# Optimization experiments

Hardware: AMD Instinct MI355X
Metric: run time of the kernel (lower is better)

The kernel has to match this reference:

```python
import jax, jax.numpy as jnp
import numpy as np

N = 50000
E = 800000
IN, H, OUT = 128, 96, 64
BN_EPS = 1e-5


def setup_inputs() -> dict:
    key = jax.random.key(0)
    ks = jax.random.split(key, 16)
    x = jax.random.normal(ks[0], (N, IN), dtype=jnp.float32)
    edge_index = jax.random.randint(ks[1], (2, E), 0, N, dtype=jnp.int64)
    edge_weight = jax.random.uniform(ks[2], (E,), dtype=jnp.float32)
    def lin(k, fo, fi):
        # PyG glorot-ish init
        s = 1.0 / np.sqrt(fi)
        return jax.random.uniform(k, (fo, fi), minval=-s, maxval=s, dtype=jnp.float32)
    W1, b1 = lin(ks[3], H, IN), jnp.zeros((H,), jnp.float32)
    W2, b2 = lin(ks[4], H, H), jnp.zeros((H,), jnp.float32)
    W3, b3 = lin(ks[5], OUT, H), jnp.zeros((OUT,), jnp.float32)
    g1 = jnp.ones((H,), jnp.float32); beta1 = jnp.zeros((H,), jnp.float32)
    m1 = 0.1 * jax.random.normal(ks[6], (H,), dtype=jnp.float32)
    v1 = jnp.abs(1.0 + 0.1 * jax.random.normal(ks[7], (H,), dtype=jnp.float32))
    g2 = jnp.ones((H,), jnp.float32); beta2 = jnp.zeros((H,), jnp.float32)
    m2 = 0.1 * jax.random.normal(ks[8], (H,), dtype=jnp.float32)
    v2 = jnp.abs(1.0 + 0.1 * jax.random.normal(ks[9], (H,), dtype=jnp.float32))
    return dict(x=x, edge_index=edge_index, edge_weight=edge_weight,
                W1=W1, b1=b1, W2=W2, b2=b2, W3=W3, b3=b3,
                g1=g1, beta1=beta1, m1=m1, v1=v1,
                g2=g2, beta2=beta2, m2=m2, v2=v2)


def gcn_norm(edge_index, edge_weight, n):
    # PyG gcn_norm with add_self_loops=True, fill_value=1.0
    loop = jnp.arange(n, dtype=edge_index.dtype)
    row = jnp.concatenate([edge_index[0], loop])  # sources
    col = jnp.concatenate([edge_index[1], loop])  # targets
    ew = jnp.concatenate([edge_weight, jnp.ones((n,), edge_weight.dtype)])
    deg = jax.ops.segment_sum(ew, col, num_segments=n)
    dis = jnp.where(deg > 0, jax.lax.rsqrt(deg), 0.0)  # inf -> 0 masked_fill
    norm = dis[row] * ew * dis[col]
    return row, col, norm


def gcn_conv(x, row, col, norm, W, b, n):
    xw = x @ W.T                       # [N, F_out] dense transform first
    msg = norm[:, None] * xw[row]      # [E+N, F_out] gather + edge scale
    out = jax.ops.segment_sum(msg, col, num_segments=n)  # scatter-add
    return out + b


def bn_eval(x, gamma, beta, mean, var):
    return (x - mean) * jax.lax.rsqrt(var + BN_EPS) * gamma + beta


def reference(x, edge_index, edge_weight, W1, b1, W2, b2, W3, b3,
              g1, beta1, m1, v1, g2, beta2, m2, v2):
    n = x.shape[0]
    row, col, norm = gcn_norm(edge_index, edge_weight, n)  # cached=True: shared
    h = gcn_conv(x, row, col, norm, W1, b1, n)
    h = jax.nn.relu(bn_eval(h, g1, beta1, m1, v1))
    h = gcn_conv(h, row, col, norm, W2, b2, n)
    h = jax.nn.relu(bn_eval(h, g2, beta2, m2, v2))
    out = gcn_conv(h, row, col, norm, W3, b3, n)
    return out
```

## Files before the change

### kernel.cpp

```cpp
#include <hip/hip_runtime.h>
#include <hip/hip_fp16.h>


constexpr float BN_EPS = 1e-5f;
constexpr float DEG_SCALE = 131072.0f;
constexpr float INV_DEG_SCALE = 1.0f / 131072.0f;
constexpr float NORM_SCALE = 32768.0f;
constexpr float INV_NORM_SCALE = 1.0f / 32768.0f;

typedef _Float16 f16x8 __attribute__((ext_vector_type(8)));
typedef float f32x4 __attribute__((ext_vector_type(4)));


template <int K, int F, bool F32X, bool F32W>
__device__ __forceinline__ void gemm_block(const void* __restrict__ Xin,
                                           const void* __restrict__ Win,
                                           _Float16* __restrict__ Y,
                                           int n0b, int tid, int n,
                                           _Float16* lds) {
    constexpr int KT = K / 32;
    constexpr int FT = F / 16;
    constexpr int LROW = (F == 96) ? 104 : 72;
    int wave = tid >> 6;
    int lane = tid & 63;
    int quad = lane >> 4;
    int r = lane & 15;
    int n0 = n0b + wave * 16;
    bool active = (n0 < n);

    if (active) {
        f16x8 a[KT];
        if (F32X) {
            const float* xr = (const float*)Xin + (size_t)(n0 + r) * K + quad * 8;
#pragma unroll
            for (int kt = 0; kt < KT; ++kt) {
                float4 v0 = *(const float4*)(xr + kt * 32);
                float4 v1 = *(const float4*)(xr + kt * 32 + 4);
                f16x8 t = {(_Float16)v0.x, (_Float16)v0.y, (_Float16)v0.z, (_Float16)v0.w,
                           (_Float16)v1.x, (_Float16)v1.y, (_Float16)v1.z, (_Float16)v1.w};
                a[kt] = t;
            }
        } else {
            const f16x8* xr = (const f16x8*)((const _Float16*)Xin + (size_t)(n0 + r) * K + quad * 8);
#pragma unroll
            for (int kt = 0; kt < KT; ++kt) a[kt] = xr[kt * 4];
        }

        f32x4 acc[FT];
#pragma unroll
        for (int ft = 0; ft < FT; ++ft) acc[ft] = (f32x4){0.f, 0.f, 0.f, 0.f};

#pragma unroll
        for (int kt = 0; kt < KT; ++kt) {
#pragma unroll
            for (int ft = 0; ft < FT; ++ft) {
                f16x8 b;
                if (F32W) {
                    const float* wr = (const float*)Win + (size_t)(ft * 16 + r) * K + kt * 32 + quad * 8;
                    float4 v0 = *(const float4*)wr;
                    float4 v1 = *(const float4*)(wr + 4);
                    f16x8 t = {(_Float16)v0.x, (_Float16)v0.y, (_Float16)v0.z, (_Float16)v0.w,
                               (_Float16)v1.x, (_Float16)v1.y, (_Float16)v1.z, (_Float16)v1.w};
                    b = t;
                } else {
                    b = *(const f16x8*)((const _Float16*)Win + (size_t)(ft * 16 + r) * K + kt * 32 + quad * 8);
                }
                acc[ft] = __builtin_amdgcn_mfma_f32_16x16x32_f16(a[kt], b, acc[ft], 0, 0, 0);
            }
        }

#pragma unroll
        for (int ft = 0; ft < FT; ++ft) {
#pragma unroll
            for (int reg = 0; reg < 4; ++reg) {
                int lr = wave * 16 + quad * 4 + reg;
                lds[(size_t)lr * LROW + ft * 16 + r] = (_Float16)acc[ft][reg];
            }
        }
    }
    __syncthreads();

    constexpr int CPR = F / 8;
    constexpr int TOTAL = 64 * CPR;
    for (int i = tid; i < TOTAL; i += 256) {
        int row = i / CPR, c = i - row * CPR;
        int grow = n0b + row;
        if (grow < n)
            *(uint4*)(Y + (size_t)grow * F + c * 8) =
                *(const uint4*)(lds + (size_t)row * LROW + c * 8);
    }
}

template <int K, int F>
__global__ __launch_bounds__(256) void k_gemm(const _Float16* __restrict__ X,
                                              const _Float16* __restrict__ Wh,
                                              _Float16* __restrict__ Y, int n) {
    __shared__ _Float16 lds[64 * 104];
    gemm_block<K, F, false, false>(X, Wh, Y, blockIdx.x * 64, threadIdx.x, n, lds);
}


__global__ __launch_bounds__(256) void k_mega(
    const int* __restrict__ row_idx, const int* __restrict__ col_idx,
    const float* __restrict__ ew,
    unsigned long long* packed, unsigned char* rank, int e_cnt, int pair_b,
    int t1, int t2,
    const float* __restrict__ x, const float* __restrict__ W1,
    _Float16* __restrict__ bufA, int n,
    const float* __restrict__ W2, const float* __restrict__ W3,
    _Float16* __restrict__ w2h, _Float16* __restrict__ w3h,
    int w2n4, int w3n4) {
    __shared__ _Float16 lds[64 * 104];
    int b = blockIdx.x;
    if (b < 2 * pair_b) {
        int q = b >> 1;
        if ((b & 1) == 0) {
#pragma unroll
            for (int j = 0; j < 4; ++j) {
                int e = q * 1024 + j * 256 + (int)threadIdx.x;
                if (e < e_cnt) {
                    int c = col_idx[e];
                    int r = row_idx[e];
                    int t = (r >= t2) ? 2 : ((r >= t1) ? 1 : 0);
                    int sh = 24 + 10 * t;
                    unsigned wfix = (unsigned)(ew[e] * DEG_SCALE + 0.5f);
                    unsigned long long inc = (1ull << sh) | (unsigned long long)wfix;
                    unsigned long long old = atomicAdd(&packed[c], inc);
                    rank[e] = (unsigned char)((old >> sh) & 0x3FFull);
                }
            }
        } else {
            gemm_block<128, 96, true, true>(x, W1, bufA, q * 64, threadIdx.x, n, lds);
        }
    } else {
        int i = (b - 2 * pair_b) * 256 + (int)threadIdx.x;
        const float* src; _Float16* dst; int o;
        if (i < w2n4) { src = W2; dst = w2h; o = i; }
        else if (i < w2n4 + w3n4) { src = W3; dst = w3h; o = i - w2n4; }
        else return;
        float4 v = ((const float4*)src)[o];
        __half2 h0 = __floats2half2_rn(v.x, v.y);
        __half2 h1 = __floats2half2_rn(v.z, v.w);
        *(uint2*)(dst + (size_t)o * 4) = make_uint2(*(unsigned*)&h0, *(unsigned*)&h1);
    }
}


__device__ __forceinline__ int pk_cnt(unsigned long long p) {
    return (int)((p >> 24) & 0x3FF) + (int)((p >> 34) & 0x3FF) + (int)((p >> 44) & 0x3FF);
}

__global__ void k_scan1(const unsigned long long* __restrict__ packed,
                        int* bsum, float* dis, int n) {
    __shared__ int s[256];
    int i = blockIdx.x * 256 + threadIdx.x;
    int cnt = 0;
    if (i < n) {
        unsigned long long p = packed[i];
        cnt = pk_cnt(p);
        float wsum = (float)(unsigned)(p & 0xFFFFFFull) * INV_DEG_SCALE;
        dis[i] = rsqrtf(1.0f + wsum);
    }
    s[threadIdx.x] = cnt;
    __syncthreads();
    for (int off = 128; off > 0; off >>= 1) {
        if ((int)threadIdx.x < off) s[threadIdx.x] += s[threadIdx.x + off];
        __syncthreads();
    }
    if (threadIdx.x == 0) bsum[blockIdx.x] = s[0];
}

__global__ void k_scan23(const unsigned long long* __restrict__ packed,
                         const int* __restrict__ bsum,
                         int* row_ptr, int n, int e_total, int nb) {
    __shared__ int sb[256];
    __shared__ int s[256];
    int t = threadIdx.x;
    int bv = (t < nb) ? bsum[t] : 0;
    sb[t] = bv;
    __syncthreads();
    for (int off = 1; off < 256; off <<= 1) {
        int x = (t >= off) ? sb[t - off] : 0;
        __syncthreads();
        sb[t] += x;
        __syncthreads();
    }
    int boff = (blockIdx.x == 0) ? 0 : sb[blockIdx.x - 1];

    int i = blockIdx.x * 256 + t;
    int v = (i < n) ? pk_cnt(packed[i]) : 0;
    s[t] = v;
    __syncthreads();
    for (int off = 1; off < 256; off <<= 1) {
        int x = (t >= off) ? s[t - off] : 0;
        __syncthreads();
        s[t] += x;
        __syncthreads();
    }
    int ex = s[t] - v + boff;
    if (i < n) row_ptr[i] = ex;
    if (i == 0) row_ptr[n] = e_total;
}

__global__ void k_fill(const int* __restrict__ row_idx, const int* __restrict__ col_idx,
                       const float* __restrict__ ew, const float* __restrict__ dis,
                       const int* __restrict__ row_ptr, const unsigned char* __restrict__ rank,
                       const unsigned long long* __restrict__ packed,
                       unsigned* ep, int e_cnt, int t1, int t2) {
    int e = blockIdx.x * 256 + threadIdx.x;
    if (e < e_cnt) {
        int r = row_idx[e];
        int c = col_idx[e];
        unsigned long long p = packed[c];
        int c0 = (int)((p >> 24) & 0x3FF);
        int c1 = (int)((p >> 34) & 0x3FF);
        int t = (r >= t2) ? 2 : ((r >= t1) ? 1 : 0);
        int off = (t > 0 ? c0 : 0) + (t > 1 ? c1 : 0);
        float nm = dis[r] * ew[e];
        unsigned q = (unsigned)(nm * NORM_SCALE + 0.5f);
        if (q > 65535u) q = 65535u;
        ep[row_ptr[c] + off + (int)rank[e]] = ((unsigned)r << 16) | q;
    }
}


__device__ inline void cvt8(uint4 u, float* f) {
    float2 t;
    t = __half22float2(*(const __half2*)&u.x); f[0] = t.x; f[1] = t.y;
    t = __half22float2(*(const __half2*)&u.y); f[2] = t.x; f[3] = t.y;
    t = __half22float2(*(const __half2*)&u.z); f[4] = t.x; f[5] = t.y;
    t = __half22float2(*(const __half2*)&u.w); f[6] = t.x; f[7] = t.y;
}

__device__ inline void h8_acc(uint4 u, float w, float acc[8]) {
    float2 a = __half22float2(*(const __half2*)&u.x);
    float2 b = __half22float2(*(const __half2*)&u.y);
    float2 c = __half22float2(*(const __half2*)&u.z);
    float2 d = __half22float2(*(const __half2*)&u.w);
    acc[0] = fmaf(w, a.x, acc[0]); acc[1] = fmaf(w, a.y, acc[1]);
    acc[2] = fmaf(w, b.x, acc[2]); acc[3] = fmaf(w, b.y, acc[3]);
    acc[4] = fmaf(w, c.x, acc[4]); acc[5] = fmaf(w, c.y, acc[5]);
    acc[6] = fmaf(w, d.x, acc[6]); acc[7] = fmaf(w, d.y, acc[7]);
}

template <int F, bool BN, bool F32OUT>
__global__ __launch_bounds__(256) void k_aggr(
    const _Float16* __restrict__ xw, const int* __restrict__ row_ptr,
    const unsigned* __restrict__ ep,
    const float* __restrict__ dis, const float* __restrict__ bias,
    const float* __restrict__ g, const float* __restrict__ beta,
    const float* __restrict__ m, const float* __restrict__ v,
    void* __restrict__ out, int n) {
    constexpr int FQ = F / 8;
    int tg = blockIdx.x * 256 + threadIdx.x;
    int node = tg / FQ;
    int q = tg - node * FQ;
    if (node >= n) return;

    const uint4* __restrict__ base = (const uint4*)xw;

    float d = dis[node];
    float acc[8];
    {
        uint4 sv = base[(size_t)node * FQ + q];
        float t[8];
        cvt8(sv, t);
#pragma unroll
        for (int j = 0; j < 8; ++j) acc[j] = d * t[j];
    }

    int e0 = row_ptr[node], e1 = row_ptr[node + 1];
    int e = e0;
    for (; e + 8 <= e1; e += 8) {
        unsigned p0 = ep[e + 0], p1 = ep[e + 1], p2 = ep[e + 2], p3 = ep[e + 3];
        unsigned p4 = ep[e + 4], p5 = ep[e + 5], p6 = ep[e + 6], p7 = ep[e + 7];
        uint4 x0 = base[(size_t)(p0 >> 16) * FQ + q];
        uint4 x1 = base[(size_t)(p1 >> 16) * FQ + q];
        uint4 x2 = base[(size_t)(p2 >> 16) * FQ + q];
        uint4 x3 = base[(size_t)(p3 >> 16) * FQ + q];
        uint4 x4 = base[(size_t)(p4 >> 16) * FQ + q];
        uint4 x5 = base[(size_t)(p5 >> 16) * FQ + q];
        uint4 x6 = base[(size_t)(p6 >> 16) * FQ + q];
        uint4 x7 = base[(size_t)(p7 >> 16) * FQ + q];
        h8_acc(x0, (float)(p0 & 0xffffu) * INV_NORM_SCALE, acc);
        h8_acc(x1, (float)(p1 & 0xffffu) * INV_NORM_SCALE, acc);
        h8_acc(x2, (float)(p2 & 0xffffu) * INV_NORM_SCALE, acc);
        h8_acc(x3, (float)(p3 & 0xffffu) * INV_NORM_SCALE, acc);
        h8_acc(x4, (float)(p4 & 0xffffu) * INV_NORM_SCALE, acc);
        h8_acc(x5, (float)(p5 & 0xffffu) * INV_NORM_SCALE, acc);
        h8_acc(x6, (float)(p6 & 0xffffu) * INV_NORM_SCALE, acc);
        h8_acc(x7, (float)(p7 & 0xffffu) * INV_NORM_SCALE, acc);
    }
    for (; e + 4 <= e1; e += 4) {
        unsigned p0 = ep[e + 0], p1 = ep[e + 1], p2 = ep[e + 2], p3 = ep[e + 3];
        uint4 x0 = base[(size_t)(p0 >> 16) * FQ + q];
        uint4 x1 = base[(size_t)(p1 >> 16) * FQ + q];
        uint4 x2 = base[(size_t)(p2 >> 16) * FQ + q];
        uint4 x3 = base[(size_t)(p3 >> 16) * FQ + q];
        h8_acc(x0, (float)(p0 & 0xffffu) * INV_NORM_SCALE, acc);
        h8_acc(x1, (float)(p1 & 0xffffu) * INV_NORM_SCALE, acc);
        h8_acc(x2, (float)(p2 & 0xffffu) * INV_NORM_SCALE, acc);
        h8_acc(x3, (float)(p3 & 0xffffu) * INV_NORM_SCALE, acc);
    }
    for (; e < e1; ++e) {
        unsigned p = ep[e];
        uint4 xv = base[(size_t)(p >> 16) * FQ + q];
        h8_acc(xv, (float)(p & 0xffffu) * INV_NORM_SCALE, acc);
    }

    int fb = q * 8;
    const float4* bb = (const float4*)(bias + fb);
    float4 b0 = bb[0], b1 = bb[1];
    acc[0] = fmaf(acc[0], d, b0.x); acc[1] = fmaf(acc[1], d, b0.y);
    acc[2] = fmaf(acc[2], d, b0.z); acc[3] = fmaf(acc[3], d, b0.w);
    acc[4] = fmaf(acc[4], d, b1.x); acc[5] = fmaf(acc[5], d, b1.y);
    acc[6] = fmaf(acc[6], d, b1.z); acc[7] = fmaf(acc[7], d, b1.w);
    if (BN) {
#pragma unroll
        for (int j = 0; j < 8; ++j) {
            acc[j] = fmaxf((acc[j] - m[fb + j]) * rsqrtf(v[fb + j] + BN_EPS) * g[fb + j]
                           + beta[fb + j], 0.f);
        }
    }
    if (F32OUT) {
        float* op = (float*)out + (size_t)node * F + fb;
        *(float4*)(op + 0) = make_float4(acc[0], acc[1], acc[2], acc[3]);
        *(float4*)(op + 4) = make_float4(acc[4], acc[5], acc[6], acc[7]);
    } else {
        __half2 h0 = __floats2half2_rn(acc[0], acc[1]);
        __half2 h1 = __floats2half2_rn(acc[2], acc[3]);
        __half2 h2 = __floats2half2_rn(acc[4], acc[5]);
        __half2 h3 = __floats2half2_rn(acc[6], acc[7]);
        uint4 u = make_uint4(*(unsigned*)&h0, *(unsigned*)&h1,
                             *(unsigned*)&h2, *(unsigned*)&h3);
        ((uint4*)out)[(size_t)node * FQ + q] = u;
    }
}


extern "C" void kernel_launch(void* const* d_in, const int* in_sizes, int n_in,
                              void* d_out, int out_size, void* d_ws, size_t ws_size,
                              hipStream_t stream) {
    constexpr int IN = 128, H = 96, OUT = 64;

    const float* x   = (const float*)d_in[0];
    const int*   ei  = (const int*)d_in[1];
    const float* ew  = (const float*)d_in[2];
    const float* W1  = (const float*)d_in[3];
    const float* b1  = (const float*)d_in[4];
    const float* W2  = (const float*)d_in[5];
    const float* b2  = (const float*)d_in[6];
    const float* W3  = (const float*)d_in[7];
    const float* b3  = (const float*)d_in[8];
    const float* g1  = (const float*)d_in[9];
    const float* be1 = (const float*)d_in[10];
    const float* m1  = (const float*)d_in[11];
    const float* v1  = (const float*)d_in[12];
    const float* g2  = (const float*)d_in[13];
    const float* be2 = (const float*)d_in[14];
    const float* m2  = (const float*)d_in[15];
    const float* v2  = (const float*)d_in[16];

    const int N = in_sizes[0] / IN;
    const int E = in_sizes[2];
    const int* row_idx = ei;
    const int* col_idx = ei + E;
    const int T1 = N / 3, T2 = 2 * (N / 3);

    char* ws = (char*)d_ws;
    size_t off = 0;
    auto alloc = [&](size_t bytes) -> void* {
        void* p = ws + off;
        off = (off + bytes + 255) & ~(size_t)255;
        return p;
    };
    unsigned long long* packed = (unsigned long long*)alloc((size_t)N * 8);
    float*     dis     = (float*)alloc((size_t)N * 4);
    int*       row_ptr = (int*)alloc((size_t)(N + 1) * 4);
    int*       bsum    = (int*)alloc(256 * 4);
    unsigned char* rank = (unsigned char*)alloc((size_t)E);
    unsigned*  ep      = (unsigned*)alloc((size_t)E * 4);
    _Float16*  w2h     = (_Float16*)alloc((size_t)H * H * 2);
    _Float16*  w3h     = (_Float16*)alloc((size_t)OUT * H * 2);
    _Float16*  bufA    = (_Float16*)alloc((size_t)N * H * 2);
    _Float16*  bufB    = (_Float16*)alloc((size_t)N * H * 2);
    (void)ws_size; (void)n_in; (void)out_size;

    constexpr int W2N4 = H * H / 4, W3N4 = OUT * H / 4;
    const int NB = (N + 255) / 256;
    const int DEG1024 = (E + 1023) / 1024;
    const int GG = (N + 63) / 64;
    const int PAIR = (DEG1024 > GG) ? DEG1024 : GG;
    const int CVT_B = (W2N4 + W3N4 + 255) / 256;

    hipMemsetAsync(packed, 0, (size_t)N * 8, stream);
    k_mega<<<2 * PAIR + CVT_B, 256, 0, stream>>>(
        row_idx, col_idx, ew, packed, rank, E, PAIR, T1, T2,
        x, W1, bufA, N, W2, W3, w2h, w3h, W2N4, W3N4);
    k_scan1<<<NB, 256, 0, stream>>>(packed, bsum, dis, N);
    k_scan23<<<NB, 256, 0, stream>>>(packed, bsum, row_ptr, N, E, NB);
    k_fill<<<(E + 255) / 256, 256, 0, stream>>>(row_idx, col_idx, ew, dis,
                                                row_ptr, rank, packed, ep, E, T1, T2);

    const int GA96 = ((size_t)N * (H / 8) + 255) / 256;
    const int GA64 = ((size_t)N * (OUT / 8) + 255) / 256;

    k_aggr<H, true, false><<<GA96, 256, 0, stream>>>(
        bufA, row_ptr, ep, dis, b1, g1, be1, m1, v1, bufB, N);

    k_gemm<H, H><<<GG, 256, 0, stream>>>(bufB, w2h, bufA, N);
    k_aggr<H, true, false><<<GA96, 256, 0, stream>>>(
        bufA, row_ptr, ep, dis, b2, g2, be2, m2, v2, bufB, N);

    k_gemm<H, OUT><<<GG, 256, 0, stream>>>(bufB, w3h, bufA, N);
    k_aggr<OUT, false, true><<<GA64, 256, 0, stream>>>(
        bufA, row_ptr, ep, dis, b3, nullptr, nullptr, nullptr, nullptr, d_out, N);
}
```

Baseline: 258.3 us.

## Privatize degree atomics per XCC and merge partial counts in scan

The degree-counting atomics now go to one packed counter array per XCC, selected by reading the hardware XCC ID, and use workgroup-scope relaxed atomics instead of device-scope ones. Each edge records its XCC index alongside its rank. The scan kernel merges the eight partial arrays and writes per-node prefix offsets for each (third, XCC) pair, which the fill kernel uses to place edges. This is meant to avoid cross-XCC coherence traffic on contended atomics. In exchange it adds an 8x larger memset, eight reads per node in the scan, and an extra 48-byte-per-node offset table. Relying on workgroup scope for correctness across blocks on the same XCC is a risk.

```diff
diff --git a/kernel.cpp b/kernel.cpp
--- a/kernel.cpp
+++ b/kernel.cpp
@@ -103,7 +103,7 @@
 __global__ __launch_bounds__(256) void k_mega(
     const int* __restrict__ row_idx, const int* __restrict__ col_idx,
     const float* __restrict__ ew,
-    unsigned long long* packed, unsigned char* rank, int e_cnt, int pair_b,
+    unsigned long long* pk, unsigned short* rx, int e_cnt, int pair_b,
     int t1, int t2,
     const float* __restrict__ x, const float* __restrict__ W1,
     _Float16* __restrict__ bufA, int n,
@@ -115,6 +115,10 @@
     if (b < 2 * pair_b) {
         int q = b >> 1;
         if ((b & 1) == 0) {
+            unsigned xcc;
+            asm volatile("s_getreg_b32 %0, hwreg(HW_REG_XCC_ID)" : "=s"(xcc));
+            xcc &= 7u;
+            unsigned long long* mypk = pk + (size_t)xcc * n;
 #pragma unroll
             for (int j = 0; j < 4; ++j) {
                 int e = q * 1024 + j * 256 + (int)threadIdx.x;
@@ -125,8 +129,9 @@
                     int sh = 24 + 10 * t;
                     unsigned wfix = (unsigned)(ew[e] * DEG_SCALE + 0.5f);
                     unsigned long long inc = (1ull << sh) | (unsigned long long)wfix;
-                    unsigned long long old = atomicAdd(&packed[c], inc);
-                    rank[e] = (unsigned char)((old >> sh) & 0x3FFull);
+                    unsigned long long old = __hip_atomic_fetch_add(
+                        &mypk[c], inc, __ATOMIC_RELAXED, __HIP_MEMORY_SCOPE_WORKGROUP);
+                    rx[e] = (unsigned short)(((old >> sh) & 0x3FFull) | (xcc << 10));
                 }
             }
         } else {
@@ -146,31 +151,50 @@
 }
 
 
-__device__ __forceinline__ int pk_cnt(unsigned long long p) {
-    return (int)((p >> 24) & 0x3FF) + (int)((p >> 34) & 0x3FF) + (int)((p >> 44) & 0x3FF);
-}
-
-__global__ void k_scan1(const unsigned long long* __restrict__ packed,
-                        int* bsum, float* dis, int n) {
+__global__ void k_scan1(const unsigned long long* __restrict__ pk,
+                        int* bsum, float* dis, unsigned short* __restrict__ pre,
+                        int* __restrict__ cnta, int n) {
     __shared__ int s[256];
     int i = blockIdx.x * 256 + threadIdx.x;
     int cnt = 0;
     if (i < n) {
-        unsigned long long p = packed[i];
-        cnt = pk_cnt(p);
-        float wsum = (float)(unsigned)(p & 0xFFFFFFull) * INV_DEG_SCALE;
-        dis[i] = rsqrtf(1.0f + wsum);
+        unsigned wfix = 0;
+        unsigned short c[3][8];
+#pragma unroll
+        for (int k = 0; k < 8; ++k) {
+            unsigned long long p = pk[(size_t)k * n + i];
+            wfix += (unsigned)(p & 0xFFFFFFull);
+            c[0][k] = (unsigned short)((p >> 24) & 0x3FF);
+            c[1][k] = (unsigned short)((p >> 34) & 0x3FF);
+            c[2][k] = (unsigned short)((p >> 44) & 0x3FF);
+        }
+        alignas(16) unsigned short off[24];
+        unsigned run = 0;
+#pragma unroll
+        for (int t = 0; t < 3; ++t)
+#pragma unroll
+            for (int k = 0; k < 8; ++k) {
+                off[t * 8 + k] = (unsigned short)run;
+                run += c[t][k];
+            }
+        cnt = (int)run;
+        dis[i] = rsqrtf(1.0f + (float)wfix * INV_DEG_SCALE);
+        cnta[i] = cnt;
+        uint4* pd = (uint4*)(pre + (size_t)i * 24);
+        pd[0] = *(const uint4*)&off[0];
+        pd[1] = *(const uint4*)&off[8];
+        pd[2] = *(const uint4*)&off[16];
     }
     s[threadIdx.x] = cnt;
     __syncthreads();
-    for (int off = 128; off > 0; off >>= 1) {
-        if ((int)threadIdx.x < off) s[threadIdx.x] += s[threadIdx.x + off];
+    for (int off2 = 128; off2 > 0; off2 >>= 1) {
+        if ((int)threadIdx.x < off2) s[threadIdx.x] += s[threadIdx.x + off2];
         __syncthreads();
     }
     if (threadIdx.x == 0) bsum[blockIdx.x] = s[0];
 }
 
-__global__ void k_scan23(const unsigned long long* __restrict__ packed,
+__global__ void k_scan23(const int* __restrict__ cnta,
                          const int* __restrict__ bsum,
                          int* row_ptr, int n, int e_total, int nb) {
     __shared__ int sb[256];
@@ -188,7 +212,7 @@
     int boff = (blockIdx.x == 0) ? 0 : sb[blockIdx.x - 1];
 
     int i = blockIdx.x * 256 + t;
-    int v = (i < n) ? pk_cnt(packed[i]) : 0;
+    int v = (i < n) ? cnta[i] : 0;
     s[t] = v;
     __syncthreads();
     for (int off = 1; off < 256; off <<= 1) {
@@ -204,22 +228,23 @@
 
 __global__ void k_fill(const int* __restrict__ row_idx, const int* __restrict__ col_idx,
                        const float* __restrict__ ew, const float* __restrict__ dis,
-                       const int* __restrict__ row_ptr, const unsigned char* __restrict__ rank,
-                       const unsigned long long* __restrict__ packed,
+                       const int* __restrict__ row_ptr,
+                       const unsigned short* __restrict__ rx,
+                       const unsigned short* __restrict__ pre,
                        unsigned* ep, int e_cnt, int t1, int t2) {
     int e = blockIdx.x * 256 + threadIdx.x;
     if (e < e_cnt) {
         int r = row_idx[e];
         int c = col_idx[e];
-        unsigned long long p = packed[c];
-        int c0 = (int)((p >> 24) & 0x3FF);
-        int c1 = (int)((p >> 34) & 0x3FF);
         int t = (r >= t2) ? 2 : ((r >= t1) ? 1 : 0);
-        int off = (t > 0 ? c0 : 0) + (t > 1 ? c1 : 0);
+        unsigned rxv = rx[e];
+        int k = (int)(rxv >> 10);
+        int rk = (int)(rxv & 0x3FFu);
         float nm = dis[r] * ew[e];
         unsigned q = (unsigned)(nm * NORM_SCALE + 0.5f);
         if (q > 65535u) q = 65535u;
-        ep[row_ptr[c] + off + (int)rank[e]] = ((unsigned)r << 16) | q;
+        ep[row_ptr[c] + (int)pre[(size_t)c * 24 + t * 8 + k] + rk] =
+            ((unsigned)r << 16) | q;
     }
 }
 
@@ -374,11 +399,13 @@
         off = (off + bytes + 255) & ~(size_t)255;
         return p;
     };
-    unsigned long long* packed = (unsigned long long*)alloc((size_t)N * 8);
+    unsigned long long* pk = (unsigned long long*)alloc((size_t)8 * N * 8);
     float*     dis     = (float*)alloc((size_t)N * 4);
     int*       row_ptr = (int*)alloc((size_t)(N + 1) * 4);
     int*       bsum    = (int*)alloc(256 * 4);
-    unsigned char* rank = (unsigned char*)alloc((size_t)E);
+    int*       cnta    = (int*)alloc((size_t)N * 4);
+    unsigned short* rx = (unsigned short*)alloc((size_t)E * 2);
+    unsigned short* pre = (unsigned short*)alloc((size_t)N * 24 * 2);
     unsigned*  ep      = (unsigned*)alloc((size_t)E * 4);
     _Float16*  w2h     = (_Float16*)alloc((size_t)H * H * 2);
     _Float16*  w3h     = (_Float16*)alloc((size_t)OUT * H * 2);
@@ -393,14 +420,14 @@
     const int PAIR = (DEG1024 > GG) ? DEG1024 : GG;
     const int CVT_B = (W2N4 + W3N4 + 255) / 256;
 
-    hipMemsetAsync(packed, 0, (size_t)N * 8, stream);
+    hipMemsetAsync(pk, 0, (size_t)8 * N * 8, stream);
     k_mega<<<2 * PAIR + CVT_B, 256, 0, stream>>>(
-        row_idx, col_idx, ew, packed, rank, E, PAIR, T1, T2,
+        row_idx, col_idx, ew, pk, rx, E, PAIR, T1, T2,
         x, W1, bufA, N, W2, W3, w2h, w3h, W2N4, W3N4);
-    k_scan1<<<NB, 256, 0, stream>>>(packed, bsum, dis, N);
-    k_scan23<<<NB, 256, 0, stream>>>(packed, bsum, row_ptr, N, E, NB);
+    k_scan1<<<NB, 256, 0, stream>>>(pk, bsum, dis, pre, cnta, N);
+    k_scan23<<<NB, 256, 0, stream>>>(cnta, bsum, row_ptr, N, E, NB);
     k_fill<<<(E + 255) / 256, 256, 0, stream>>>(row_idx, col_idx, ew, dis,
-                                                row_ptr, rank, packed, ep, E, T1, T2);
+                                                row_ptr, rx, pre, ep, E, T1, T2);
 
     const int GA96 = ((size_t)N * (H / 8) + 255) / 256;
     const int GA64 = ((size_t)N * (OUT / 8) + 255) / 256;
```

Measured after the change: 266.2 us. 3.0% more time.

## Fuse aggregation+BN+ReLU with following dense GEMM in one kernel

Applied to the files above, without the earlier changes.

Merges each layer's sparse aggregation (with bias, batchnorm, ReLU) and the next layer's weight multiply into one kernel. Each 192-thread block aggregates 16 nodes into LDS, then one wave runs MFMA against the fp16 weights and writes the transformed rows. This removes two GEMM launches and the global round trip of the intermediate hidden activations. In exchange, blocks are small and only one wave does the matrix work, which may lower occupancy and leave the other waves idle during the MFMA phase.

```diff
diff --git a/kernel.cpp b/kernel.cpp
--- a/kernel.cpp
+++ b/kernel.cpp
@@ -89,14 +89,6 @@
             *(uint4*)(Y + (size_t)grow * F + c * 8) =
                 *(const uint4*)(lds + (size_t)row * LROW + c * 8);
     }
-}
-
-template <int K, int F>
-__global__ __launch_bounds__(256) void k_gemm(const _Float16* __restrict__ X,
-                                              const _Float16* __restrict__ Wh,
-                                              _Float16* __restrict__ Y, int n) {
-    __shared__ _Float16 lds[64 * 104];
-    gemm_block<K, F, false, false>(X, Wh, Y, blockIdx.x * 64, threadIdx.x, n, lds);
 }
 
 
@@ -243,33 +235,10 @@
     acc[6] = fmaf(w, d.x, acc[6]); acc[7] = fmaf(w, d.y, acc[7]);
 }
 
-template <int F, bool BN, bool F32OUT>
-__global__ __launch_bounds__(256) void k_aggr(
-    const _Float16* __restrict__ xw, const int* __restrict__ row_ptr,
-    const unsigned* __restrict__ ep,
-    const float* __restrict__ dis, const float* __restrict__ bias,
-    const float* __restrict__ g, const float* __restrict__ beta,
-    const float* __restrict__ m, const float* __restrict__ v,
-    void* __restrict__ out, int n) {
-    constexpr int FQ = F / 8;
-    int tg = blockIdx.x * 256 + threadIdx.x;
-    int node = tg / FQ;
-    int q = tg - node * FQ;
-    if (node >= n) return;
-
-    const uint4* __restrict__ base = (const uint4*)xw;
-
-    float d = dis[node];
-    float acc[8];
-    {
-        uint4 sv = base[(size_t)node * FQ + q];
-        float t[8];
-        cvt8(sv, t);
-#pragma unroll
-        for (int j = 0; j < 8; ++j) acc[j] = d * t[j];
-    }
-
-    int e0 = row_ptr[node], e1 = row_ptr[node + 1];
+template <int FQ>
+__device__ __forceinline__ void gather_row(const uint4* __restrict__ base,
+                                           const unsigned* __restrict__ ep,
+                                           int e0, int e1, int q, float acc[8]) {
     int e = e0;
     for (; e + 8 <= e1; e += 8) {
         unsigned p0 = ep[e + 0], p1 = ep[e + 1], p2 = ep[e + 2], p3 = ep[e + 3];
@@ -307,6 +276,125 @@
         uint4 xv = base[(size_t)(p >> 16) * FQ + q];
         h8_acc(xv, (float)(p & 0xffffu) * INV_NORM_SCALE, acc);
     }
+}
+
+
+template <int FOUT>
+__global__ __launch_bounds__(192) void k_aggr_mm(
+    const _Float16* __restrict__ xw,
+    const int* __restrict__ row_ptr, const unsigned* __restrict__ ep,
+    const float* __restrict__ dis, const float* __restrict__ bias,
+    const float* __restrict__ g, const float* __restrict__ beta,
+    const float* __restrict__ m, const float* __restrict__ v,
+    const _Float16* __restrict__ Wh,
+    _Float16* __restrict__ Y, int n) {
+    constexpr int LROW = 104;
+    __shared__ _Float16 lds[16 * LROW];
+    int tid = (int)threadIdx.x;
+    int n0b = blockIdx.x * 16;
+    int nl = tid / 12;
+    int q = tid - nl * 12;
+    int node = n0b + nl;
+    const uint4* __restrict__ base = (const uint4*)xw;
+
+    if (node < n) {
+        float d = dis[node];
+        float acc[8];
+        {
+            uint4 sv = base[(size_t)node * 12 + q];
+            float t[8];
+            cvt8(sv, t);
+#pragma unroll
+            for (int j = 0; j < 8; ++j) acc[j] = d * t[j];
+        }
+        gather_row<12>(base, ep, row_ptr[node], row_ptr[node + 1], q, acc);
+
+        int fb = q * 8;
+        const float4* bb = (const float4*)(bias + fb);
+        float4 b0 = bb[0], b1 = bb[1];
+        acc[0] = fmaf(acc[0], d, b0.x); acc[1] = fmaf(acc[1], d, b0.y);
+        acc[2] = fmaf(acc[2], d, b0.z); acc[3] = fmaf(acc[3], d, b0.w);
+        acc[4] = fmaf(acc[4], d, b1.x); acc[5] = fmaf(acc[5], d, b1.y);
+        acc[6] = fmaf(acc[6], d, b1.z); acc[7] = fmaf(acc[7], d, b1.w);
+#pragma unroll
+        for (int j = 0; j < 8; ++j) {
+            acc[j] = fmaxf((acc[j] - m[fb + j]) * rsqrtf(v[fb + j] + BN_EPS) * g[fb + j]
+                           + beta[fb + j], 0.f);
+        }
+        __half2 h0 = __floats2half2_rn(acc[0], acc[1]);
+        __half2 h1 = __floats2half2_rn(acc[2], acc[3]);
+        __half2 h2 = __floats2half2_rn(acc[4], acc[5]);
+        __half2 h3 = __floats2half2_rn(acc[6], acc[7]);
+        *(uint4*)(lds + (size_t)nl * LROW + fb) =
+            make_uint4(*(unsigned*)&h0, *(unsigned*)&h1, *(unsigned*)&h2, *(unsigned*)&h3);
+    }
+    __syncthreads();
+
+    constexpr int FT = FOUT / 16;
+    f32x4 cacc[FT];
+    int lane = tid, quad = tid >> 4, r = tid & 15;
+    if (tid < 64) {
+        f16x8 a[3];
+#pragma unroll
+        for (int kt = 0; kt < 3; ++kt)
+            a[kt] = *(const f16x8*)(lds + (size_t)r * LROW + kt * 32 + quad * 8);
+#pragma unroll
+        for (int ft = 0; ft < FT; ++ft) cacc[ft] = (f32x4){0.f, 0.f, 0.f, 0.f};
+#pragma unroll
+        for (int kt = 0; kt < 3; ++kt) {
+#pragma unroll
+            for (int ft = 0; ft < FT; ++ft) {
+                f16x8 b = *(const f16x8*)(Wh + (size_t)(ft * 16 + r) * 96 + kt * 32 + quad * 8);
+                cacc[ft] = __builtin_amdgcn_mfma_f32_16x16x32_f16(a[kt], b, cacc[ft], 0, 0, 0);
+            }
+        }
+    }
+    __syncthreads();
+    if (tid < 64) {
+#pragma unroll
+        for (int ft = 0; ft < FT; ++ft) {
+#pragma unroll
+            for (int reg = 0; reg < 4; ++reg) {
+                lds[(size_t)(quad * 4 + reg) * LROW + ft * 16 + r] = (_Float16)cacc[ft][reg];
+            }
+        }
+    }
+    (void)lane;
+    __syncthreads();
+
+    constexpr int CPR = FOUT / 8;
+    for (int i = tid; i < 16 * CPR; i += 192) {
+        int row = i / CPR, c = i - row * CPR;
+        int grow = n0b + row;
+        if (grow < n)
+            *(uint4*)(Y + (size_t)grow * FOUT + c * 8) =
+                *(const uint4*)(lds + (size_t)row * LROW + c * 8);
+    }
+}
+
+
+__global__ __launch_bounds__(256) void k_aggr3(
+    const _Float16* __restrict__ xw, const int* __restrict__ row_ptr,
+    const unsigned* __restrict__ ep,
+    const float* __restrict__ dis, const float* __restrict__ bias,
+    float* __restrict__ out, int n) {
+    constexpr int FQ = 8;
+    int tg = blockIdx.x * 256 + threadIdx.x;
+    int node = tg / FQ;
+    int q = tg - node * FQ;
+    if (node >= n) return;
+
+    const uint4* __restrict__ base = (const uint4*)xw;
+    float d = dis[node];
+    float acc[8];
+    {
+        uint4 sv = base[(size_t)node * FQ + q];
+        float t[8];
+        cvt8(sv, t);
+#pragma unroll
+        for (int j = 0; j < 8; ++j) acc[j] = d * t[j];
+    }
+    gather_row<FQ>(base, ep, row_ptr[node], row_ptr[node + 1], q, acc);
 
     int fb = q * 8;
     const float4* bb = (const float4*)(bias + fb);
@@ -315,26 +403,10 @@
     acc[2] = fmaf(acc[2], d, b0.z); acc[3] = fmaf(acc[3], d, b0.w);
     acc[4] = fmaf(acc[4], d, b1.x); acc[5] = fmaf(acc[5], d, b1.y);
     acc[6] = fmaf(acc[6], d, b1.z); acc[7] = fmaf(acc[7], d, b1.w);
-    if (BN) {
-#pragma unroll
-        for (int j = 0; j < 8; ++j) {
-            acc[j] = fmaxf((acc[j] - m[fb + j]) * rsqrtf(v[fb + j] + BN_EPS) * g[fb + j]
-                           + beta[fb + j], 0.f);
-        }
-    }
-    if (F32OUT) {
-        float* op = (float*)out + (size_t)node * F + fb;
-        *(float4*)(op + 0) = make_float4(acc[0], acc[1], acc[2], acc[3]);
-        *(float4*)(op + 4) = make_float4(acc[4], acc[5], acc[6], acc[7]);
-    } else {
-        __half2 h0 = __floats2half2_rn(acc[0], acc[1]);
-        __half2 h1 = __floats2half2_rn(acc[2], acc[3]);
-        __half2 h2 = __floats2half2_rn(acc[4], acc[5]);
-        __half2 h3 = __floats2half2_rn(acc[6], acc[7]);
-        uint4 u = make_uint4(*(unsigned*)&h0, *(unsigned*)&h1,
-                             *(unsigned*)&h2, *(unsigned*)&h3);
-        ((uint4*)out)[(size_t)node * FQ + q] = u;
-    }
+
+    float* op = out + (size_t)node * 64 + fb;
+    *(float4*)(op + 0) = make_float4(acc[0], acc[1], acc[2], acc[3]);
+    *(float4*)(op + 4) = make_float4(acc[4], acc[5], acc[6], acc[7]);
 }
 
 
@@ -402,17 +474,14 @@
     k_fill<<<(E + 255) / 256, 256, 0, stream>>>(row_idx, col_idx, ew, dis,
                                                 row_ptr, rank, packed, ep, E, T1, T2);
 
-    const int GA96 = ((size_t)N * (H / 8) + 255) / 256;
+    const int GF = (N + 15) / 16;
     const int GA64 = ((size_t)N * (OUT / 8) + 255) / 256;
 
-    k_aggr<H, true, false><<<GA96, 256, 0, stream>>>(
-        bufA, row_ptr, ep, dis, b1, g1, be1, m1, v1, bufB, N);
-
-    k_gemm<H, H><<<GG, 256, 0, stream>>>(bufB, w2h, bufA, N);
-    k_aggr<H, true, false><<<GA96, 256, 0, stream>>>(
-        bufA, row_ptr, ep, dis, b2, g2, be2, m2, v2, bufB, N);
-
-    k_gemm<H, OUT><<<GG, 256, 0, stream>>>(bufB, w3h, bufA, N);
-    k_aggr<OUT, false, true><<<GA64, 256, 0, stream>>>(
-        bufA, row_ptr, ep, dis, b3, nullptr, nullptr, nullptr, nullptr, d_out, N);
-}
+    k_aggr_mm<H><<<GF, 192, 0, stream>>>(
+        bufA, row_ptr, ep, dis, b1, g1, be1, m1, v1, w2h, bufB, N);
+
+    k_aggr_mm<OUT><<<GF, 192, 0, stream>>>(
+        bufB, row_ptr, ep, dis, b2, g2, be2, m2, v2, w3h, bufA, N);
+
+    k_aggr3<<<GA64, 256, 0, stream>>>(bufA, row_ptr, ep, dis, b3, (float*)d_out, N);
+}
```

Measured after the change: 253.4 us. No clear change (-1.9%).
